# Kernel tuning notes

Hardware: AMD Instinct MI355X
Metric: run time of the kernel (lower is better)

## Reference

```python
import jax, jax.numpy as jnp
import numpy as np

T, D_IN, D_OUT, E, K = 4096, 1024, 1024, 8, 2
H = max(D_IN, D_OUT) * 4  # 4096, per nbHidden = max(nbIn, nbOut) * 4


def setup_inputs() -> dict:
    key = jax.random.key(0)
    ks = jax.random.split(key, 12)
    s = 0.02
    return {
        "x": jax.random.normal(ks[0], (T, D_IN), dtype=jnp.float32),
        "noise": jax.random.normal(ks[1], (T, E), dtype=jnp.float32),
        "gate_w": jax.random.normal(ks[2], (D_IN, E), dtype=jnp.float32) * s,
        "gate_b": jnp.zeros((E,), dtype=jnp.float32),
        "noise_w": jax.random.normal(ks[3], (D_IN, E), dtype=jnp.float32) * s,
        "noise_b": jnp.zeros((E,), dtype=jnp.float32),
        "w1": jax.random.normal(ks[4], (E, D_IN, H), dtype=jnp.float32) * s,
        "b1": jnp.zeros((E, H), dtype=jnp.float32),
        "w2": jax.random.normal(ks[5], (E, H, D_OUT), dtype=jnp.float32) * s,
        "b2": jnp.zeros((E, D_OUT), dtype=jnp.float32),
    }


def reference(x, noise, gate_w, gate_b, noise_w, noise_b, w1, b1, w2, b2):
    # Noisy gating: gate(x) + randn * softplus(noise(x))
    logits = (x @ gate_w + gate_b) + noise * jax.nn.softplus(x @ noise_w + noise_b)  # [T, E]
    topk_vals, topk_idx = jax.lax.top_k(logits, K)          # [T, K]
    gate_prob = jax.nn.softmax(topk_vals, axis=1)           # softmax over selected K logits
    rows = jnp.arange(x.shape[0])[:, None]
    weights = jnp.zeros((x.shape[0], E), dtype=x.dtype).at[rows, topk_idx].set(gate_prob)  # [T, E]

    # Dense path (memMode=False): run every expert MLP on all tokens, masked combine.
    h = jax.nn.relu(jnp.einsum("ti,eih->teh", x, w1) + b1[None])   # [T, E, H]
    expert_out = jnp.einsum("teh,eho->teo", h, w2) + b2[None]       # [T, E, O]
    x_out = jnp.einsum("te,teo->to", weights, expert_out)           # [T, O]
    return x_out, weights
```

## Files before the change

### kernel.cpp

```cpp
#include <hip/hip_runtime.h>

#define T_TOK 4096
#define DIN   1024
#define DOUT  1024
#define NEXP  8
#define HDIM  4096
#define RCAP  9216
#define MT128 80

typedef float f32x4 __attribute__((ext_vector_type(4)));
typedef short bf16x8 __attribute__((ext_vector_type(8)));
typedef unsigned short u16x4 __attribute__((ext_vector_type(4)));
typedef unsigned short u16x8 __attribute__((ext_vector_type(8)));

__device__ __forceinline__ float bf2f(unsigned short u) {
    union { unsigned int i; float f; } v; v.i = ((unsigned int)u) << 16; return v.f;
}
__device__ __forceinline__ unsigned short f2bf(float f) {
    union { unsigned int i; float f; } v; v.f = f;
    unsigned int r = v.i + 0x7FFFu + ((v.i >> 16) & 1u);
    return (unsigned short)(r >> 16);
}

__global__ __launch_bounds__(64) void gating_kernel(
    const float* __restrict__ x, const float* __restrict__ noise,
    const float* __restrict__ gw, const float* __restrict__ gb,
    const float* __restrict__ nw, const float* __restrict__ nb,
    float* __restrict__ wout,
    int* __restrict__ tok_e, float* __restrict__ tok_p)
{
    int t = blockIdx.x;
    int lane = threadIdx.x;
    const float* xr = x + (size_t)t * DIN;
    double ag[NEXP], an[NEXP];
#pragma unroll
    for (int e = 0; e < NEXP; ++e) { ag[e] = 0.0; an[e] = 0.0; }
    for (int d = lane; d < DIN; d += 64) {
        double xv = (double)xr[d];
        const f32x4* g4 = (const f32x4*)(gw + (size_t)d * NEXP);
        const f32x4* n4 = (const f32x4*)(nw + (size_t)d * NEXP);
        f32x4 ga = g4[0], gbv = g4[1], na = n4[0], nbv = n4[1];
#pragma unroll
        for (int j = 0; j < 4; ++j) {
            ag[j]     += xv * (double)ga[j];
            ag[4 + j] += xv * (double)gbv[j];
            an[j]     += xv * (double)na[j];
            an[4 + j] += xv * (double)nbv[j];
        }
    }
#pragma unroll
    for (int e = 0; e < NEXP; ++e) {
        double g = ag[e], n = an[e];
#pragma unroll
        for (int m = 32; m > 0; m >>= 1) { g += __shfl_xor(g, m); n += __shfl_xor(n, m); }
        ag[e] = g; an[e] = n;
    }
    double lg[NEXP];
#pragma unroll
    for (int e = 0; e < NEXP; ++e) {
        double z = an[e] + (double)nb[e];
        double sp = fmax(z, 0.0) + log1p(exp(-fabs(z)));
        lg[e] = ag[e] + (double)gb[e] + (double)noise[(size_t)t * NEXP + e] * sp;
    }
    int i0 = 0; double v0 = lg[0];
#pragma unroll
    for (int e = 1; e < NEXP; ++e) if (lg[e] > v0) { v0 = lg[e]; i0 = e; }
    int i1 = -1; double v1 = -1.0e300;
#pragma unroll
    for (int e = 0; e < NEXP; ++e) if (e != i0 && lg[e] > v1) { v1 = lg[e]; i1 = e; }
    double d1 = exp(v1 - v0);
    float p0 = (float)(1.0 / (1.0 + d1));
    float p1 = (float)(d1 / (1.0 + d1));
    if (lane < NEXP) {
        float wv = (lane == i0) ? p0 : ((lane == i1) ? p1 : 0.0f);
        wout[(size_t)t * NEXP + lane] = wv;
    }
    if (lane == 0) {
        tok_e[2 * t] = i0;     tok_e[2 * t + 1] = i1;
        tok_p[2 * t] = p0;     tok_p[2 * t + 1] = p1;
    }
}

__global__ __launch_bounds__(256) void scan_kernel(
    const int* __restrict__ tok_e, int* __restrict__ tok_slot, int* __restrict__ cnt)
{
    __shared__ int wsum[4];
    int e = blockIdx.x;
    int tid = threadIdx.x;
    int wv = tid >> 6;
    int lane = tid & 63;
    int base = 0;
    for (int c = 0; c < 2 * T_TOK; c += 256) {
        int i = c + tid;
        int m = (tok_e[i] == e) ? 1 : 0;
        unsigned long long bal = __ballot(m);
        int before = __popcll(bal & ((1ull << lane) - 1ull));
        if (lane == 0) wsum[wv] = __popcll(bal);
        __syncthreads();
        int woff = 0;
#pragma unroll
        for (int w = 0; w < 4; ++w) if (w < wv) woff += wsum[w];
        if (m) tok_slot[i] = base + woff + before;
        int tot = wsum[0] + wsum[1] + wsum[2] + wsum[3];
        __syncthreads();
        base += tot;
    }
    if (tid == 0) cnt[e] = base;
}

__global__ void prefix_kernel(const int* __restrict__ cnt, int* __restrict__ poff,
                              int* __restrict__ t2e, int* __restrict__ trow)
{
    if (threadIdx.x != 0 || blockIdx.x != 0) return;
    int base = 0, a = 0;
    for (int e = 0; e < NEXP; ++e) {
        poff[e] = base;
        int c = cnt[e];
        int nt = (c + 127) >> 7;
        for (int i = 0; i < nt; ++i) { t2e[a] = e; trow[a] = base + (i << 7); ++a; }
        base += nt << 7;
    }
    for (; a < MT128; ++a) { t2e[a] = -1; trow[a] = 0; }
}

__global__ __launch_bounds__(256) void gather_kernel(
    const float* __restrict__ x, const int* __restrict__ tok_e,
    const int* __restrict__ tok_slot, const int* __restrict__ poff,
    unsigned short* __restrict__ Xg)
{
    int b = blockIdx.x;
    int t = b >> 1, k = b & 1;
    int e = tok_e[2 * t + k];
    int row = poff[e] + tok_slot[2 * t + k];
    int c = threadIdx.x << 2;
    f32x4 v = *(const f32x4*)(x + (size_t)t * DIN + c);
    u16x4 o;
#pragma unroll
    for (int j = 0; j < 4; ++j) o[j] = f2bf(v[j]);
    *(u16x4*)(Xg + (size_t)row * DIN + c) = o;
}

__global__ __launch_bounds__(256) void convw_kernel(
    const float* __restrict__ W, unsigned short* __restrict__ Wt, int K, int N)
{
    __shared__ float tile[64][65];
    int e = blockIdx.x;
    int k0 = blockIdx.y << 6;
    int n0 = blockIdx.z << 6;
    int tid = threadIdx.x;
    const float* src = W + ((size_t)e * K + k0) * N + n0;
    int r = tid >> 4, c4 = (tid & 15) << 2;
#pragma unroll
    for (int i = 0; i < 4; ++i) {
        f32x4 v = *(const f32x4*)(src + (size_t)(r + (i << 4)) * N + c4);
        *(f32x4*)(&tile[r + (i << 4)][c4]) = v;
    }
    __syncthreads();
    unsigned short* dst = Wt + ((size_t)e * N + n0) * K + k0;
#pragma unroll
    for (int i = 0; i < 2; ++i) {
        int u = (i << 8) + tid;
        int n = u >> 3, kk = (u & 7) << 3;
        u16x8 o;
#pragma unroll
        for (int q = 0; q < 8; ++q) o[q] = f2bf(tile[kk + q][n]);
        *(u16x8*)(dst + (size_t)n * K + kk) = o;
    }
}

__global__ __launch_bounds__(256, 2) void gemm64_kernel(
    const unsigned short* __restrict__ A, int lda,
    const unsigned short* __restrict__ Bt, int ldb, int N, int KLEN,
    unsigned short* __restrict__ C,
    const float* __restrict__ bias,
    const int* __restrict__ t2e, const int* __restrict__ trow,
    int nbshift, int relu)
{
    int nwg = gridDim.x;
    int cpx = nwg >> 3;
    int wg = ((blockIdx.x & 7) * cpx) + (blockIdx.x >> 3);
    int tileid = wg >> nbshift;
    int nb = wg & ((1 << nbshift) - 1);

    int e = t2e[tileid];
    if (e < 0) return;
    int row0 = trow[tileid];
    int n0 = nb << 7;

    __shared__ __align__(16) unsigned short As0[128 * 64];
    __shared__ __align__(16) unsigned short Bs0[128 * 64];
    __shared__ __align__(16) unsigned short As1[128 * 64];
    __shared__ __align__(16) unsigned short Bs1[128 * 64];

    int tid = threadIdx.x;
    int lane = tid & 63;
    int wv = tid >> 6;
    int wr = (wv >> 1) << 6;
    int wc = (wv & 1) << 6;

    const unsigned short* Ab = A + (size_t)row0 * lda;
    const unsigned short* Bb = Bt + ((size_t)e * N + n0) * ldb;

    f32x4 acc[4][4] = {};

    int sr_lo = tid >> 3;
    int sp = tid & 7;
    int hr = lane & 15;
    int q4 = lane >> 4;

#define STAGE(AS, BS, KT)                                                              \
    {                                                                                  \
        int kb = (KT) << 6;                                                            \
        _Pragma("unroll")                                                              \
        for (int i = 0; i < 4; ++i) {                                                  \
            int r = (i << 5) + sr_lo;                                                  \
            int col = ((sp ^ (r & 7)) << 3);                                           \
            int u = (i << 8) + tid;                                                    \
            __builtin_amdgcn_global_load_lds(                                          \
                (const __attribute__((address_space(1))) void*)(Ab + (size_t)r * lda + kb + col), \
                (__attribute__((address_space(3))) void*)(&AS[u << 3]), 16, 0, 0);     \
            __builtin_amdgcn_global_load_lds(                                          \
                (const __attribute__((address_space(1))) void*)(Bb + (size_t)r * ldb + kb + col), \
                (__attribute__((address_space(3))) void*)(&BS[u << 3]), 16, 0, 0);     \
        }                                                                              \
    }

#define COMPUTE(AS, BS)                                                                \
    {                                                                                  \
        _Pragma("unroll")                                                              \
        for (int kq = 0; kq < 2; ++kq) {                                               \
            int slog = (kq << 2) | q4;                                                 \
            bf16x8 af[4], bfv[4];                                                      \
            _Pragma("unroll")                                                          \
            for (int m = 0; m < 4; ++m) {                                              \
                int r = wr + (m << 4) + hr;                                            \
                af[m] = *(const bf16x8*)(&AS[(r << 6) + ((slog ^ (r & 7)) << 3)]);     \
            }                                                                          \
            _Pragma("unroll")                                                          \
            for (int n = 0; n < 4; ++n) {                                              \
                int r = wc + (n << 4) + hr;                                            \
                bfv[n] = *(const bf16x8*)(&BS[(r << 6) + ((slog ^ (r & 7)) << 3)]);    \
            }                                                                          \
            _Pragma("unroll")                                                          \
            for (int m = 0; m < 4; ++m)                                                \
                _Pragma("unroll")                                                      \
                for (int n = 0; n < 4; ++n)                                            \
                    acc[m][n] = __builtin_amdgcn_mfma_f32_16x16x32_bf16(af[m], bfv[n], acc[m][n], 0, 0, 0); \
        }                                                                              \
    }

    int nkt = KLEN >> 6;
    STAGE(As0, Bs0, 0);
    __syncthreads();
    for (int kt = 0; kt < nkt; kt += 2) {
        STAGE(As1, Bs1, kt + 1);
        COMPUTE(As0, Bs0);
        __syncthreads();
        if (kt + 2 < nkt) STAGE(As0, Bs0, kt + 2);
        COMPUTE(As1, Bs1);
        __syncthreads();
    }
#undef STAGE
#undef COMPUTE

    int rq = q4 << 2;
    int cl = hr;
#pragma unroll
    for (int n = 0; n < 4; ++n) {
        int col = wc + (n << 4) + cl;
        float bv = bias[(size_t)e * N + n0 + col];
#pragma unroll
        for (int m = 0; m < 4; ++m) {
#pragma unroll
            for (int r = 0; r < 4; ++r) {
                int row = wr + (m << 4) + rq + r;
                float v = acc[m][n][r] + bv;
                if (relu) v = fmaxf(v, 0.0f);
                C[(size_t)(row0 + row) * N + n0 + col] = f2bf(v);
            }
        }
    }
}

__global__ __launch_bounds__(256) void combine_kernel(
    const unsigned short* __restrict__ O, const int* __restrict__ tok_e,
    const int* __restrict__ tok_slot, const float* __restrict__ tok_p,
    const int* __restrict__ poff, float* __restrict__ xout)
{
    int t = blockIdx.x;
    int e0 = tok_e[2 * t], e1 = tok_e[2 * t + 1];
    int r0 = poff[e0] + tok_slot[2 * t];
    int r1 = poff[e1] + tok_slot[2 * t + 1];
    float p0 = tok_p[2 * t], p1 = tok_p[2 * t + 1];
    int c = threadIdx.x << 2;
    u16x4 a = *(const u16x4*)(O + (size_t)r0 * DOUT + c);
    u16x4 b = *(const u16x4*)(O + (size_t)r1 * DOUT + c);
    f32x4 r;
#pragma unroll
    for (int j = 0; j < 4; ++j) r[j] = p0 * bf2f(a[j]) + p1 * bf2f(b[j]);
    *(f32x4*)(xout + (size_t)t * DOUT + c) = r;
}

extern "C" void kernel_launch(void* const* d_in, const int* in_sizes, int n_in,
                              void* d_out, int out_size, void* d_ws, size_t ws_size,
                              hipStream_t stream)
{
    const float* x     = (const float*)d_in[0];
    const float* noise = (const float*)d_in[1];
    const float* gw    = (const float*)d_in[2];
    const float* gb    = (const float*)d_in[3];
    const float* nw    = (const float*)d_in[4];
    const float* nb    = (const float*)d_in[5];
    const float* w1    = (const float*)d_in[6];
    const float* b1    = (const float*)d_in[7];
    const float* w2    = (const float*)d_in[8];
    const float* b2    = (const float*)d_in[9];
    float* xout = (float*)d_out;
    float* wout = xout + (size_t)T_TOK * DOUT;

    char* ws = (char*)d_ws;
    int*   cnt      = (int*)(ws + 0);
    int*   poff     = (int*)(ws + 256);
    int*   t2e      = (int*)(ws + 512);
    int*   trow     = (int*)(ws + 1024);
    int*   tok_e    = (int*)(ws + 2048);
    int*   tok_slot = (int*)(ws + 34816);
    float* tok_p    = (float*)(ws + 67584);
    size_t oXg = 104448;
    unsigned short* Xg  = (unsigned short*)(ws + oXg);
    unsigned short* O   = Xg;
    size_t oH  = oXg + (size_t)RCAP * DIN * 2;
    unsigned short* H   = (unsigned short*)(ws + oH);
    size_t oW1 = oH + (size_t)RCAP * HDIM * 2;
    unsigned short* W1t = (unsigned short*)(ws + oW1);
    size_t oW2 = oW1 + (size_t)NEXP * HDIM * DIN * 2;
    unsigned short* W2t = (unsigned short*)(ws + oW2);

    gating_kernel<<<T_TOK, 64, 0, stream>>>(x, noise, gw, gb, nw, nb,
                                            wout, tok_e, tok_p);
    scan_kernel<<<NEXP, 256, 0, stream>>>(tok_e, tok_slot, cnt);
    prefix_kernel<<<1, 1, 0, stream>>>(cnt, poff, t2e, trow);
    gather_kernel<<<2 * T_TOK, 256, 0, stream>>>(x, tok_e, tok_slot, poff, Xg);
    convw_kernel<<<dim3(NEXP, DIN / 64, HDIM / 64), 256, 0, stream>>>(w1, W1t, DIN, HDIM);
    convw_kernel<<<dim3(NEXP, HDIM / 64, DOUT / 64), 256, 0, stream>>>(w2, W2t, HDIM, DOUT);
    gemm64_kernel<<<MT128 * 32, 256, 0, stream>>>(
        Xg, DIN, W1t, DIN, HDIM, DIN, H, b1, t2e, trow, 5, 1);
    gemm64_kernel<<<MT128 * 8, 256, 0, stream>>>(
        H, HDIM, W2t, HDIM, DOUT, HDIM, O, b2, t2e, trow, 3, 0);
    combine_kernel<<<T_TOK, 256, 0, stream>>>(O, tok_e, tok_slot, tok_p, poff, xout);
}
```

Before: 390.5 us.

## Halve GEMM K-tile to 32 to double occupancy with new LDS swizzle

The grouped expert GEMM now stages 32-wide K slices instead of 64, halving shared memory per block and raising the launch-bounds occupancy hint from 2 to 4 blocks per CU. The staging and fragment-read addressing switches to a new XOR swizzle suited to 32-element rows, with each wave loading its own 16-row chunks. The goal is more resident waves to hide memory latency. In exchange there are twice as many barriers and stage iterations per K, with fewer MFMAs between syncs, and register pressure may be tighter under the new bound.

```diff
diff --git a/kernel.cpp b/kernel.cpp
--- a/kernel.cpp
+++ b/kernel.cpp
@@ -168,7 +168,7 @@
     }
 }
 
-__global__ __launch_bounds__(256, 2) void gemm64_kernel(
+__global__ __launch_bounds__(256, 4) void gemm32db_kernel(
     const unsigned short* __restrict__ A, int lda,
     const unsigned short* __restrict__ Bt, int ldb, int N, int KLEN,
     unsigned short* __restrict__ C,
@@ -187,10 +187,10 @@
     int row0 = trow[tileid];
     int n0 = nb << 7;
 
-    __shared__ __align__(16) unsigned short As0[128 * 64];
-    __shared__ __align__(16) unsigned short Bs0[128 * 64];
-    __shared__ __align__(16) unsigned short As1[128 * 64];
-    __shared__ __align__(16) unsigned short Bs1[128 * 64];
+    __shared__ __align__(16) unsigned short As0[128 * 32];
+    __shared__ __align__(16) unsigned short Bs0[128 * 32];
+    __shared__ __align__(16) unsigned short As1[128 * 32];
+    __shared__ __align__(16) unsigned short Bs1[128 * 32];
 
     int tid = threadIdx.x;
     int lane = tid & 63;
@@ -203,53 +203,44 @@
 
     f32x4 acc[4][4] = {};
 
-    int sr_lo = tid >> 3;
-    int sp = tid & 7;
+    int srow = lane >> 2;
+    int skc = (((lane & 3) ^ ((lane >> 3) & 3)) << 3);
     int hr = lane & 15;
-    int q4 = lane >> 4;
+    int kfrag = (((lane >> 4) ^ ((lane >> 1) & 3)) << 3);
 
 #define STAGE(AS, BS, KT)                                                              \
     {                                                                                  \
-        int kb = (KT) << 6;                                                            \
+        int kb = (KT) << 5;                                                            \
         _Pragma("unroll")                                                              \
-        for (int i = 0; i < 4; ++i) {                                                  \
-            int r = (i << 5) + sr_lo;                                                  \
-            int col = ((sp ^ (r & 7)) << 3);                                           \
-            int u = (i << 8) + tid;                                                    \
+        for (int j = 0; j < 2; ++j) {                                                  \
+            int c = wv + (j << 2);                                                     \
+            int r = (c << 4) + srow;                                                   \
             __builtin_amdgcn_global_load_lds(                                          \
-                (const __attribute__((address_space(1))) void*)(Ab + (size_t)r * lda + kb + col), \
-                (__attribute__((address_space(3))) void*)(&AS[u << 3]), 16, 0, 0);     \
+                (const __attribute__((address_space(1))) void*)(Ab + (size_t)r * lda + kb + skc), \
+                (__attribute__((address_space(3))) void*)(&AS[c << 9]), 16, 0, 0);     \
             __builtin_amdgcn_global_load_lds(                                          \
-                (const __attribute__((address_space(1))) void*)(Bb + (size_t)r * ldb + kb + col), \
-                (__attribute__((address_space(3))) void*)(&BS[u << 3]), 16, 0, 0);     \
+                (const __attribute__((address_space(1))) void*)(Bb + (size_t)r * ldb + kb + skc), \
+                (__attribute__((address_space(3))) void*)(&BS[c << 9]), 16, 0, 0);     \
         }                                                                              \
     }
 
 #define COMPUTE(AS, BS)                                                                \
     {                                                                                  \
+        bf16x8 af[4], bfv[4];                                                          \
         _Pragma("unroll")                                                              \
-        for (int kq = 0; kq < 2; ++kq) {                                               \
-            int slog = (kq << 2) | q4;                                                 \
-            bf16x8 af[4], bfv[4];                                                      \
+        for (int m = 0; m < 4; ++m)                                                    \
+            af[m] = *(const bf16x8*)(&AS[((wr + (m << 4) + hr) << 5) + kfrag]);        \
+        _Pragma("unroll")                                                              \
+        for (int n = 0; n < 4; ++n)                                                    \
+            bfv[n] = *(const bf16x8*)(&BS[((wc + (n << 4) + hr) << 5) + kfrag]);       \
+        _Pragma("unroll")                                                              \
+        for (int m = 0; m < 4; ++m)                                                    \
             _Pragma("unroll")                                                          \
-            for (int m = 0; m < 4; ++m) {                                              \
-                int r = wr + (m << 4) + hr;                                            \
-                af[m] = *(const bf16x8*)(&AS[(r << 6) + ((slog ^ (r & 7)) << 3)]);     \
-            }                                                                          \
-            _Pragma("unroll")                                                          \
-            for (int n = 0; n < 4; ++n) {                                              \
-                int r = wc + (n << 4) + hr;                                            \
-                bfv[n] = *(const bf16x8*)(&BS[(r << 6) + ((slog ^ (r & 7)) << 3)]);    \
-            }                                                                          \
-            _Pragma("unroll")                                                          \
-            for (int m = 0; m < 4; ++m)                                                \
-                _Pragma("unroll")                                                      \
-                for (int n = 0; n < 4; ++n)                                            \
-                    acc[m][n] = __builtin_amdgcn_mfma_f32_16x16x32_bf16(af[m], bfv[n], acc[m][n], 0, 0, 0); \
-        }                                                                              \
-    }
-
-    int nkt = KLEN >> 6;
+            for (int n = 0; n < 4; ++n)                                                \
+                acc[m][n] = __builtin_amdgcn_mfma_f32_16x16x32_bf16(af[m], bfv[n], acc[m][n], 0, 0, 0); \
+    }
+
+    int nkt = KLEN >> 5;
     STAGE(As0, Bs0, 0);
     __syncthreads();
     for (int kt = 0; kt < nkt; kt += 2) {
@@ -263,7 +254,7 @@
 #undef STAGE
 #undef COMPUTE
 
-    int rq = q4 << 2;
+    int rq = (lane >> 4) << 2;
     int cl = hr;
 #pragma unroll
     for (int n = 0; n < 4; ++n) {
@@ -343,9 +334,9 @@
     gather_kernel<<<2 * T_TOK, 256, 0, stream>>>(x, tok_e, tok_slot, poff, Xg);
     convw_kernel<<<dim3(NEXP, DIN / 64, HDIM / 64), 256, 0, stream>>>(w1, W1t, DIN, HDIM);
     convw_kernel<<<dim3(NEXP, HDIM / 64, DOUT / 64), 256, 0, stream>>>(w2, W2t, HDIM, DOUT);
-    gemm64_kernel<<<MT128 * 32, 256, 0, stream>>>(
+    gemm32db_kernel<<<MT128 * 32, 256, 0, stream>>>(
         Xg, DIN, W1t, DIN, HDIM, DIN, H, b1, t2e, trow, 5, 1);
-    gemm64_kernel<<<MT128 * 8, 256, 0, stream>>>(
+    gemm32db_kernel<<<MT128 * 8, 256, 0, stream>>>(
         H, HDIM, W2t, HDIM, DOUT, HDIM, O, b2, t2e, trow, 3, 0);
     combine_kernel<<<T_TOK, 256, 0, stream>>>(O, tok_e, tok_slot, tok_p, poff, xout);
 }
```

After: 374.8 us. -4.0%, faster.
